# Kernel tuning notes

Measured on AMD Instinct MI355X. Metric: run time of the kernel, lower is better.

The kernel has to match this reference:

```python
import jax, jax.numpy as jnp
import numpy as np

EMBED = 128
NLOC = 360
N, T, F = 4, 128, 512


def setup_inputs() -> dict:
    key = jax.random.key(0)
    ks = jax.random.split(key, 8)
    s = 1.0 / np.sqrt(EMBED)
    return {
        "value": jax.random.normal(ks[0], (N, T, F, EMBED), jnp.float32),
        "key": jax.random.normal(ks[1], (N, T, F, EMBED), jnp.float32),
        "query": jax.random.normal(ks[2], (N, T, F, EMBED), jnp.float32),
        # nn.Linear weights: [out_features, in_features], applied as x @ W.T
        "Wv": jax.random.uniform(ks[3], (EMBED, EMBED), jnp.float32, -s, s),
        "Wk": jax.random.uniform(ks[4], (EMBED, EMBED), jnp.float32, -s, s),
        "Wq": jax.random.uniform(ks[5], (EMBED, EMBED), jnp.float32, -s, s),
        "Wo": jax.random.uniform(ks[6], (NLOC, EMBED), jnp.float32, -s, s),
        "bo": jax.random.uniform(ks[7], (NLOC,), jnp.float32, -s, s),
    }


def reference(value, key, query, Wv, Wk, Wq, Wo, bo):
    # Linear projections (no bias), torch Linear => x @ W.T
    values = jnp.einsum("ntve,fe->ntvf", value, Wv)
    keys = jnp.einsum("ntke,fe->ntkf", key, Wk)
    queries = jnp.einsum("ntqe,fe->ntqf", query, Wq)
    # energy: contract over time t; per-channel attention across freq bins
    energy = jnp.einsum("ntqe,ntke->neqk", queries, keys)  # [N,E,Fq,Fk]
    scale = EMBED ** 0.5
    attention = jax.nn.softmax(energy / scale, axis=3)
    # weighted sum: contract attention's k axis with values' freq axis
    out = jnp.einsum("neqk,ntve->ntqe", attention, values)  # [N,T,Fq,E]
    # output projection to Nloc
    return jnp.einsum("ntqe,le->ntql", out, Wo) + bo
```

## Files before the change

### kernel.cpp

```cpp
#include <hip/hip_runtime.h>

#define NT 512
#define FD 512
#define ED 128
#define LD 360


__global__ __launch_bounds__(256) void kB_reduce_project(
    const float* __restrict__ value,
    const float* __restrict__ Wv,
    const float* __restrict__ Wo,
    const float* __restrict__ bo,
    float* __restrict__ G)
{
    const int nt  = blockIdx.x;
    const int tid = threadIdx.x;

    __shared__ float sRed[8][ED];
    __shared__ float sS[ED];
    __shared__ float sP[ED];

    const float* base = value + (size_t)nt * FD * ED;

    const int c4 = (tid & 31) * 4;
    const int vg = tid >> 5;
    float4 acc; acc.x = 0.f; acc.y = 0.f; acc.z = 0.f; acc.w = 0.f;
    for (int v = vg; v < FD; v += 8) {
        const float4 r = *(const float4*)&base[(size_t)v * ED + c4];
        acc.x += r.x; acc.y += r.y; acc.z += r.z; acc.w += r.w;
    }
    *(float4*)&sRed[vg][c4] = acc;
    __syncthreads();

    if (tid < ED) {
        float s = 0.f;
        #pragma unroll
        for (int g = 0; g < 8; ++g) s += sRed[g][tid];
        sS[tid] = s;
    }
    __syncthreads();

    if (tid < ED) {
        const float* wr = Wv + (size_t)tid * ED;
        float p = 0.f;
        #pragma unroll
        for (int c = 0; c < ED; c += 4) {
            const float4 w4 = *(const float4*)&wr[c];
            const float4 s4 = *(const float4*)&sS[c];
            p += w4.x * s4.x + w4.y * s4.y + w4.z * s4.z + w4.w * s4.w;
        }
        sP[tid] = p;
    }
    __syncthreads();

    for (int l = tid; l < LD; l += 256) {
        const float* wr = Wo + (size_t)l * ED;
        float g = bo[l];
        #pragma unroll
        for (int e = 0; e < ED; e += 4) {
            const float4 w4 = *(const float4*)&wr[e];
            const float4 p4 = *(const float4*)&sP[e];
            g += w4.x * p4.x + w4.y * p4.y + w4.z * p4.z + w4.w * p4.w;
        }
        G[(size_t)nt * LD + l] = g;
    }
}

__global__ __launch_bounds__(256) void kC_broadcast(
    const float* __restrict__ G,
    float* __restrict__ out)
{
    const int nt  = blockIdx.x;
    const int qc  = blockIdx.y;
    const int tid = threadIdx.x;

    __shared__ float sG[LD];
    for (int l = tid; l < LD; l += 256) sG[l] = G[(size_t)nt * LD + l];
    __syncthreads();

    const float4* sG4 = (const float4*)sG;
    float4* ob4 = (float4*)(out + ((size_t)nt * FD + (size_t)qc * 64) * LD);
    for (int idx = tid; idx < 64 * 90; idx += 256) {
        const int r = idx % 90;
        ob4[idx] = sG4[r];
    }
}

extern "C" void kernel_launch(void* const* d_in, const int* in_sizes, int n_in,
                              void* d_out, int out_size, void* d_ws, size_t ws_size,
                              hipStream_t stream) {
    (void)in_sizes; (void)n_in; (void)out_size; (void)ws_size;
    const float* value = (const float*)d_in[0];
    const float* Wv    = (const float*)d_in[3];
    const float* Wo    = (const float*)d_in[6];
    const float* bo    = (const float*)d_in[7];
    float* out = (float*)d_out;
    float* G   = (float*)d_ws;

    kB_reduce_project<<<dim3(NT), dim3(256), 0, stream>>>(value, Wv, Wo, bo, G);
    kC_broadcast<<<dim3(NT, FD / 64), dim3(256), 0, stream>>>(G, out);
}
```

Baseline: 131.4 us.

## Fuse reduce-project and broadcast kernels into one 512-thread kernel

Merges the per-(n,t) value reduction, the two small projections and the output broadcast into a single kernel with 512 threads per block. The projected row stays in shared memory instead of making a round trip through a global workspace, and the second launch goes away. The broadcast is restructured so each wave writes whole 360-float rows with float4 stores. In exchange there are only 512 blocks in total, so each block's read phase and large write phase run back to back with less grid-level parallelism for the store-bound part.

```diff
diff --git a/kernel.cpp b/kernel.cpp
--- a/kernel.cpp
+++ b/kernel.cpp
@@ -6,27 +6,29 @@
 #define LD 360
 
 
-__global__ __launch_bounds__(256) void kB_reduce_project(
+__global__ __launch_bounds__(512) void fused_attn(
     const float* __restrict__ value,
     const float* __restrict__ Wv,
     const float* __restrict__ Wo,
     const float* __restrict__ bo,
-    float* __restrict__ G)
+    float* __restrict__ out)
 {
     const int nt  = blockIdx.x;
     const int tid = threadIdx.x;
 
-    __shared__ float sRed[8][ED];
+    __shared__ float sRed[16][ED];
     __shared__ float sS[ED];
     __shared__ float sP[ED];
-
-    const float* base = value + (size_t)nt * FD * ED;
+    __shared__ float sG[LD];
 
     const int c4 = (tid & 31) * 4;
     const int vg = tid >> 5;
+    const float* base = value + (size_t)nt * FD * ED;
+
     float4 acc; acc.x = 0.f; acc.y = 0.f; acc.z = 0.f; acc.w = 0.f;
-    for (int v = vg; v < FD; v += 8) {
-        const float4 r = *(const float4*)&base[(size_t)v * ED + c4];
+    #pragma unroll 8
+    for (int i = 0; i < 32; ++i) {
+        const float4 r = *(const float4*)&base[(size_t)(vg + 16 * i) * ED + c4];
         acc.x += r.x; acc.y += r.y; acc.z += r.z; acc.w += r.w;
     }
     *(float4*)&sRed[vg][c4] = acc;
@@ -35,7 +37,7 @@
     if (tid < ED) {
         float s = 0.f;
         #pragma unroll
-        for (int g = 0; g < 8; ++g) s += sRed[g][tid];
+        for (int g = 0; g < 16; ++g) s += sRed[g][tid];
         sS[tid] = s;
     }
     __syncthreads();
@@ -53,50 +55,43 @@
     }
     __syncthreads();
 
-    for (int l = tid; l < LD; l += 256) {
-        const float* wr = Wo + (size_t)l * ED;
-        float g = bo[l];
+    if (tid < LD) {
+        const float* wr = Wo + (size_t)tid * ED;
+        float g = bo[tid];
         #pragma unroll
         for (int e = 0; e < ED; e += 4) {
             const float4 w4 = *(const float4*)&wr[e];
             const float4 p4 = *(const float4*)&sP[e];
             g += w4.x * p4.x + w4.y * p4.y + w4.z * p4.z + w4.w * p4.w;
         }
-        G[(size_t)nt * LD + l] = g;
+        sG[tid] = g;
     }
-}
-
-__global__ __launch_bounds__(256) void kC_broadcast(
-    const float* __restrict__ G,
-    float* __restrict__ out)
-{
-    const int nt  = blockIdx.x;
-    const int qc  = blockIdx.y;
-    const int tid = threadIdx.x;
-
-    __shared__ float sG[LD];
-    for (int l = tid; l < LD; l += 256) sG[l] = G[(size_t)nt * LD + l];
     __syncthreads();
 
+    const int wave = tid >> 6;
+    const int lane = tid & 63;
     const float4* sG4 = (const float4*)sG;
-    float4* ob4 = (float4*)(out + ((size_t)nt * FD + (size_t)qc * 64) * LD);
-    for (int idx = tid; idx < 64 * 90; idx += 256) {
-        const int r = idx % 90;
-        ob4[idx] = sG4[r];
+    float4 rA = sG4[lane];
+    float4 rB; rB.x = 0.f; rB.y = 0.f; rB.z = 0.f; rB.w = 0.f;
+    if (lane < 26) rB = sG4[64 + lane];
+
+    float* obase = out + (size_t)nt * FD * LD;
+    for (int r = wave; r < FD; r += 8) {
+        float4* row = (float4*)(obase + (size_t)r * LD);
+        row[lane] = rA;
+        if (lane < 26) row[64 + lane] = rB;
     }
 }
 
 extern "C" void kernel_launch(void* const* d_in, const int* in_sizes, int n_in,
                               void* d_out, int out_size, void* d_ws, size_t ws_size,
                               hipStream_t stream) {
-    (void)in_sizes; (void)n_in; (void)out_size; (void)ws_size;
+    (void)in_sizes; (void)n_in; (void)out_size; (void)d_ws; (void)ws_size;
     const float* value = (const float*)d_in[0];
     const float* Wv    = (const float*)d_in[3];
     const float* Wo    = (const float*)d_in[6];
     const float* bo    = (const float*)d_in[7];
     float* out = (float*)d_out;
-    float* G   = (float*)d_ws;
 
-    kB_reduce_project<<<dim3(NT), dim3(256), 0, stream>>>(value, Wv, Wo, bo, G);
-    kC_broadcast<<<dim3(NT, FD / 64), dim3(256), 0, stream>>>(G, out);
+    fused_attn<<<dim3(NT), dim3(512), 0, stream>>>(value, Wv, Wo, bo, out);
 }
```

New measurement: 112.4 us, median of 2. 14.4% less time.
